# Kernel optimization log

Hardware: AMD Instinct MI355X
Metric: run time of the kernel (lower is better)

The kernel has to match this reference:

```python
import jax, jax.numpy as jnp
import numpy as np

# Camera / renderer constants from the original forward():
#   renderer.eye = get_points_from_angles(2.732, 0, 90); Renderer defaults.
DIST, ELEV, AZIM = 2.732, 0.0, 90.0
VIEW_ANGLE = 30.0          # neural_renderer Renderer default viewing angle (deg)
S = 256                    # image_size (Renderer default)
SIGMA = 3e-3               # softness of the differentiable edge test
EPS = 1e-12


def _normalize(v):
    return v / (jnp.linalg.norm(v) + EPS)


def _project(vertices):
    """look_at + perspective projection -> 2D NDC coords. vertices: [B,N,3]."""
    e = jnp.deg2rad(jnp.float32(ELEV))
    a = jnp.deg2rad(jnp.float32(AZIM))
    eye = jnp.array([DIST * jnp.cos(e) * jnp.sin(a),
                     DIST * jnp.sin(e),
                     -DIST * jnp.cos(e) * jnp.cos(a)], dtype=jnp.float32)
    at = jnp.zeros(3, jnp.float32)
    up = jnp.array([0.0, 1.0, 0.0], jnp.float32)
    zax = _normalize(at - eye)
    xax = _normalize(jnp.cross(up, zax))
    yax = jnp.cross(zax, xax)
    R = jnp.stack([xax, yax, zax])                 # [3,3], rows = camera axes
    v_cam = (vertices - eye) @ R.T                 # [B,N,3]
    w = jnp.tan(jnp.deg2rad(jnp.float32(VIEW_ANGLE)))
    z = jnp.maximum(v_cam[..., 2], 1e-2)           # guard behind-camera verts
    return v_cam[..., :2] / (z[..., None] * w)     # [B,N,2]


def _rasterize_one(xy, faces):
    """Soft silhouette rasterization. xy: [N,2], faces: [F,3] -> [S,S]."""
    tri = xy[faces]                                # [F,3,2]
    ps = (jnp.arange(S, dtype=jnp.float32) + 0.5) / S * 2.0 - 1.0
    px = ps[None, :]                               # x along columns  [1,S]
    py = -ps[:, None]                              # y down rows      [S,1]
    v0, v1, v2 = tri[:, 0], tri[:, 1], tri[:, 2]   # each [F,2]
    # winding sign so "inside" => positive signed edge distance
    area = ((v1[:, 0] - v0[:, 0]) * (v2[:, 1] - v0[:, 1])
            - (v1[:, 1] - v0[:, 1]) * (v2[:, 0] - v0[:, 0]))
    s = jnp.where(area >= 0, 1.0, -1.0)            # [F]
    d = jnp.full((faces.shape[0], S, S), jnp.inf, jnp.float32)
    for a_, b_ in ((v0, v1), (v1, v2), (v2, v0)):
        e = b_ - a_                                # [F,2]
        c = (e[:, 0, None, None] * (py[None] - a_[:, 1, None, None])
             - e[:, 1, None, None] * (px[None] - a_[:, 0, None, None]))  # [F,S,S]
        d = jnp.minimum(d, s[:, None, None] * c /
                        (jnp.linalg.norm(e, axis=-1)[:, None, None] + EPS))
    prob = jax.nn.sigmoid(d / SIGMA)               # per-face coverage [F,S,S]
    return 1.0 - jnp.prod(1.0 - prob, axis=0)      # union over faces  [S,S]


def _render_silhouettes(vertices, faces):
    xy = _project(vertices)                        # [B,N,2]
    return jax.vmap(_rasterize_one)(xy, faces)     # [B,S,S]


def setup_inputs() -> dict:
    key = jax.random.key(0)
    k1, k2, k3 = jax.random.split(key, 3)
    N, F = 512, 1024
    # mesh vertices scaled so the object sits in front of the camera at d=2.732
    vertices = 0.3 * jax.random.normal(k1, (1, N, 3), jnp.float32)
    faces = jax.random.randint(k2, (1, F, 3), 0, N, jnp.int32)
    image_ref = jax.random.uniform(k3, (1, S, S), dtype=jnp.float32)
    return {"vertices": vertices, "image_ref": image_ref, "faces": faces}


def reference(vertices, image_ref, faces):
    sil = _render_silhouettes(vertices, faces)     # [B,S,S]
    return jnp.sum((sil - image_ref) ** 2)
```

## Files before the change

### kernel.cpp

```cpp
#include <hip/hip_runtime.h>
#include <math.h>

#define NF 1024
#define IMS 256
#define TILE 8
#define NT 1024
constexpr float SIGMA = 0.003f;
constexpr float LOG2E = 1.4426950408889634f;
constexpr float PXSZ = 2.0f / (float)IMS;
constexpr float TILE_R = 3.5f * PXSZ;

#if __has_builtin(__builtin_amdgcn_exp2f)
#define EXP2(x) __builtin_amdgcn_exp2f(x)
#else
#define EXP2(x) exp2f(x)
#endif

__global__ __launch_bounds__(256) void fused_kernel(const float* __restrict__ verts,
                                                    const int* __restrict__ faces,
                                                    const float* __restrict__ img,
                                                    float* __restrict__ out) {
    __shared__ float4 fc[NF * 3];
    __shared__ unsigned short slist[NF];
    __shared__ float part[4][64];
    __shared__ int cnt, cov;
    int t = threadIdx.x;
    int tile = blockIdx.x;
    int ti = tile >> 5, tj = tile & 31;
    if (t == 0) { cnt = 0; cov = 0; }
    __syncthreads();

    const float deg2rad = 0.017453292519943295f;
    float e = 0.0f * deg2rad, a = 90.0f * deg2rad;
    float ce = cosf(e), se = sinf(e), ca = cosf(a), sa = sinf(a);
    float ex = 2.732f * ce * sa, ey = 2.732f * se, ez = -2.732f * ce * ca;
    float zn = sqrtf(ex*ex + ey*ey + ez*ez) + 1e-12f;
    float zx = -ex/zn, zy = -ey/zn, zz = -ez/zn;
    float cx = 1.0f*zz, cyv = 0.0f, cz = -1.0f*zx;
    float xn = sqrtf(cx*cx + cyv*cyv + cz*cz) + 1e-12f;
    float xax_x = cx/xn, xax_y = cyv/xn, xax_z = cz/xn;
    float yx = zy*xax_z - zz*xax_y;
    float yy = zz*xax_x - zx*xax_z;
    float yz = zx*xax_y - zy*xax_x;
    float w = tanf(30.0f * deg2rad);

    float cxn = ((float)(tj * TILE) + 4.0f) * PXSZ - 1.0f;
    float cyn = -(((float)(ti * TILE) + 4.0f) * PXSZ - 1.0f);

    #pragma unroll
    for (int k = 0; k < NF / 256; ++k) {
        int f = t + 256 * k;
        int idx[3] = {faces[f*3+0], faces[f*3+1], faces[f*3+2]};
        float P[3][2];
        #pragma unroll
        for (int kk = 0; kk < 3; ++kk) {
            float vx = verts[idx[kk]*3+0] - ex;
            float vy = verts[idx[kk]*3+1] - ey;
            float vz = verts[idx[kk]*3+2] - ez;
            float camx = xax_x*vx + xax_y*vy + xax_z*vz;
            float camy = yx*vx + yy*vy + yz*vz;
            float camz = zx*vx + zy*vy + zz*vz;
            float z = fmaxf(camz, 0.01f);
            float invzw = 1.0f / (z * w);
            P[kk][0] = camx * invzw;
            P[kk][1] = camy * invzw;
        }
        float area = (P[1][0]-P[0][0])*(P[2][1]-P[0][1]) - (P[1][1]-P[0][1])*(P[2][0]-P[0][0]);
        float s = (area >= 0.0f) ? 1.0f : -1.0f;
        float o[9];
        #pragma unroll
        for (int kk = 0; kk < 3; ++kk) {
            float x0 = P[kk][0],       y0 = P[kk][1];
            float x1 = P[(kk+1)%3][0], y1 = P[(kk+1)%3][1];
            float ex_ = x1 - x0, ey_ = y1 - y0;
            float len = sqrtf(ex_*ex_ + ey_*ey_);
            float inv = s * (LOG2E / SIGMA) / (len + 1e-12f);
            o[kk*3+0] = -ey_ * inv;
            o[kk*3+1] =  ex_ * inv;
            o[kk*3+2] = (ey_*x0 - ex_*y0) * inv;
        }
        fc[f*3+0] = make_float4(o[0], o[1], o[2], o[3]);
        fc[f*3+1] = make_float4(o[4], o[5], o[6], o[7]);
        fc[f*3+2] = make_float4(o[8], 0.0f, 0.0f, 0.0f);
        float d0 = fmaf(o[0], cxn, fmaf(o[1], cyn, o[2]));
        float r0 = (fabsf(o[0]) + fabsf(o[1])) * TILE_R;
        float d1 = fmaf(o[3], cxn, fmaf(o[4], cyn, o[5]));
        float r1 = (fabsf(o[3]) + fabsf(o[4])) * TILE_R;
        float d2 = fmaf(o[6], cxn, fmaf(o[7], cyn, o[8]));
        float r2 = (fabsf(o[6]) + fabsf(o[7])) * TILE_R;
        float t_hi = fminf(d0 + r0, fminf(d1 + r1, d2 + r2));
        float t_lo = fminf(d0 - r0, fminf(d1 - r1, d2 - r2));
        if (t_lo > 130.0f) atomicOr(&cov, 1);
        else if (t_hi > -26.0f) {
            int pos = atomicAdd(&cnt, 1);
            slist[pos] = (unsigned short)f;
        }
    }
    __syncthreads();

    int lane = t & 63, wave = t >> 6;
    int pi = ti * TILE + (lane >> 3);
    int pj = tj * TILE + (lane & 7);
    float px = ((float)pj + 0.5f) * PXSZ - 1.0f;
    float py = -(((float)pi + 0.5f) * PXSZ - 1.0f);
    float prod = 1.0f;
    int covered = cov;
    if (!covered) {
        int len = cnt;
        int it = 0;
        for (int j = wave; j < len; j += 4) {
            int f = (int)slist[j];
            float4 c0 = fc[f*3+0];
            float4 c1 = fc[f*3+1];
            float4 c2 = fc[f*3+2];
            float d0 = fmaf(c0.x, px, fmaf(c0.y, py, c0.z));
            float d1 = fmaf(c0.w, px, fmaf(c1.x, py, c1.y));
            float d2 = fmaf(c1.z, px, fmaf(c1.w, py, c2.x));
            float tm = fminf(d0, fminf(d1, d2));
            float ef = EXP2(tm);
            prod *= __builtin_amdgcn_rcpf(1.0f + ef);
            if ((++it & 7) == 0 && __ballot(prod > 0.0f) == 0ull) break;
        }
    }
    part[wave][lane] = prod;
    __syncthreads();

    if (wave == 0) {
        float pr = covered ? 0.0f
                 : part[0][lane] * part[1][lane] * part[2][lane] * part[3][lane];
        float sil = 1.0f - pr;
        float diff = sil - img[pi * IMS + pj];
        float v = diff * diff;
        #pragma unroll
        for (int o = 32; o > 0; o >>= 1) v += __shfl_down(v, o);
        if (lane == 0) atomicAdd(out, v);
    }
}

extern "C" void kernel_launch(void* const* d_in, const int* in_sizes, int n_in,
                              void* d_out, int out_size, void* d_ws, size_t ws_size,
                              hipStream_t stream) {
    const float* verts = (const float*)d_in[0];
    const float* img   = (const float*)d_in[1];
    const int*   faces = (const int*)d_in[2];
    float* out = (float*)d_out;

    hipMemsetAsync(out, 0, sizeof(float), stream);
    fused_kernel<<<NT, 256, 0, stream>>>(verts, faces, img, out);
}
```

Measured before the change: 34.72 us.

## Project vertices once into shared memory and compact surviving face coefficients

Each block now projects all 512 vertices once into shared memory, so the per-face setup no longer gathers and reprojects three vertices from global memory per face. Edge coefficients are written only for faces that pass the tile test, stored compacted in structure-of-arrays shared buffers. This removes the index indirection in the rasterization loop, and all lanes of a wave read the same address, which is a broadcast. It adds an extra barrier and nine scalar shared stores per surviving face in exchange for the cheaper vertex loads and compacted reads.

Result: faster. 30.25 us (-12.9%).

```diff
diff --git a/kernel.cpp b/kernel.cpp
--- a/kernel.cpp
+++ b/kernel.cpp
@@ -1,6 +1,7 @@
 #include <hip/hip_runtime.h>
 #include <math.h>
 
+#define NV 512
 #define NF 1024
 #define IMS 256
 #define TILE 8
@@ -20,8 +21,8 @@
                                                     const int* __restrict__ faces,
                                                     const float* __restrict__ img,
                                                     float* __restrict__ out) {
-    __shared__ float4 fc[NF * 3];
-    __shared__ unsigned short slist[NF];
+    __shared__ float sxy[2][NV];
+    __shared__ float sfc[9][NF];
     __shared__ float part[4][64];
     __shared__ int cnt, cov;
     int t = threadIdx.x;
@@ -44,27 +45,33 @@
     float yz = zx*xax_y - zy*xax_x;
     float w = tanf(30.0f * deg2rad);
 
+    #pragma unroll
+    for (int k = 0; k < NV / 256; ++k) {
+        int i = t + 256 * k;
+        float vx = verts[i*3+0] - ex;
+        float vy = verts[i*3+1] - ey;
+        float vz = verts[i*3+2] - ez;
+        float camx = xax_x*vx + xax_y*vy + xax_z*vz;
+        float camy = yx*vx + yy*vy + yz*vz;
+        float camz = zx*vx + zy*vy + zz*vz;
+        float z = fmaxf(camz, 0.01f);
+        float invzw = 1.0f / (z * w);
+        sxy[0][i] = camx * invzw;
+        sxy[1][i] = camy * invzw;
+    }
+    __syncthreads();
+
     float cxn = ((float)(tj * TILE) + 4.0f) * PXSZ - 1.0f;
     float cyn = -(((float)(ti * TILE) + 4.0f) * PXSZ - 1.0f);
 
     #pragma unroll
     for (int k = 0; k < NF / 256; ++k) {
         int f = t + 256 * k;
-        int idx[3] = {faces[f*3+0], faces[f*3+1], faces[f*3+2]};
+        int i0 = faces[f*3+0], i1 = faces[f*3+1], i2 = faces[f*3+2];
         float P[3][2];
-        #pragma unroll
-        for (int kk = 0; kk < 3; ++kk) {
-            float vx = verts[idx[kk]*3+0] - ex;
-            float vy = verts[idx[kk]*3+1] - ey;
-            float vz = verts[idx[kk]*3+2] - ez;
-            float camx = xax_x*vx + xax_y*vy + xax_z*vz;
-            float camy = yx*vx + yy*vy + yz*vz;
-            float camz = zx*vx + zy*vy + zz*vz;
-            float z = fmaxf(camz, 0.01f);
-            float invzw = 1.0f / (z * w);
-            P[kk][0] = camx * invzw;
-            P[kk][1] = camy * invzw;
-        }
+        P[0][0] = sxy[0][i0]; P[0][1] = sxy[1][i0];
+        P[1][0] = sxy[0][i1]; P[1][1] = sxy[1][i1];
+        P[2][0] = sxy[0][i2]; P[2][1] = sxy[1][i2];
         float area = (P[1][0]-P[0][0])*(P[2][1]-P[0][1]) - (P[1][1]-P[0][1])*(P[2][0]-P[0][0]);
         float s = (area >= 0.0f) ? 1.0f : -1.0f;
         float o[9];
@@ -79,9 +86,6 @@
             o[kk*3+1] =  ex_ * inv;
             o[kk*3+2] = (ey_*x0 - ex_*y0) * inv;
         }
-        fc[f*3+0] = make_float4(o[0], o[1], o[2], o[3]);
-        fc[f*3+1] = make_float4(o[4], o[5], o[6], o[7]);
-        fc[f*3+2] = make_float4(o[8], 0.0f, 0.0f, 0.0f);
         float d0 = fmaf(o[0], cxn, fmaf(o[1], cyn, o[2]));
         float r0 = (fabsf(o[0]) + fabsf(o[1])) * TILE_R;
         float d1 = fmaf(o[3], cxn, fmaf(o[4], cyn, o[5]));
@@ -93,7 +97,8 @@
         if (t_lo > 130.0f) atomicOr(&cov, 1);
         else if (t_hi > -26.0f) {
             int pos = atomicAdd(&cnt, 1);
-            slist[pos] = (unsigned short)f;
+            #pragma unroll
+            for (int q = 0; q < 9; ++q) sfc[q][pos] = o[q];
         }
     }
     __syncthreads();
@@ -109,13 +114,12 @@
         int len = cnt;
         int it = 0;
         for (int j = wave; j < len; j += 4) {
-            int f = (int)slist[j];
-            float4 c0 = fc[f*3+0];
-            float4 c1 = fc[f*3+1];
-            float4 c2 = fc[f*3+2];
-            float d0 = fmaf(c0.x, px, fmaf(c0.y, py, c0.z));
-            float d1 = fmaf(c0.w, px, fmaf(c1.x, py, c1.y));
-            float d2 = fmaf(c1.z, px, fmaf(c1.w, py, c2.x));
+            float c0 = sfc[0][j], c1 = sfc[1][j], c2 = sfc[2][j];
+            float c3 = sfc[3][j], c4 = sfc[4][j], c5 = sfc[5][j];
+            float c6 = sfc[6][j], c7 = sfc[7][j], c8 = sfc[8][j];
+            float d0 = fmaf(c0, px, fmaf(c1, py, c2));
+            float d1 = fmaf(c3, px, fmaf(c4, py, c5));
+            float d2 = fmaf(c6, px, fmaf(c7, py, c8));
             float tm = fminf(d0, fminf(d1, d2));
             float ef = EXP2(tm);
             prod *= __builtin_amdgcn_rcpf(1.0f + ef);
```
